# Kernel optimization log

Measured on AMD Instinct MI355X. Metric: run time of the kernel, lower is better.

The kernel has to match this reference:

```python
import jax, jax.numpy as jnp
import numpy as np

N, E, FT_IN, HID, FT_OUT, H = 32768, 524288, 256, 256, 512, 4
C = HID // H  # per-head dim = 64


def gatv2_conv(x, edge_index, w_l, b_l, w_r, b_r, att, bias):
    """PyG GATv2Conv (eval mode, add_self_loops=True, concat=True)."""
    n = x.shape[0]
    loop = jnp.arange(n)
    src = jnp.concatenate([edge_index[0], loop])  # j (source / neighbor)
    dst = jnp.concatenate([edge_index[1], loop])  # i (target)
    x_l = (x @ w_l + b_l).reshape(n, H, C)
    x_r = (x @ w_r + b_r).reshape(n, H, C)
    e = jax.nn.leaky_relu(x_l[src] + x_r[dst], 0.2)        # [E+N, H, C]
    logits = jnp.einsum('ehc,hc->eh', e, att)              # [E+N, H]
    m = jax.ops.segment_max(logits, dst, num_segments=n)
    m = jnp.where(jnp.isfinite(m), m, 0.0)
    p = jnp.exp(logits - m[dst])
    s = jax.ops.segment_sum(p, dst, num_segments=n)
    alpha = p / (s[dst] + 1e-16)                           # scatter-softmax over in-edges
    out = jax.ops.segment_sum(alpha[:, :, None] * x_l[src], dst, num_segments=n)
    return out.reshape(n, H * C) + bias


def gelu(x):
    return jax.nn.gelu(x, approximate=False)  # torch nn.GELU default (erf)


def setup_inputs() -> dict:
    key = jax.random.key(0)
    ks = jax.random.split(key, 24)
    sc = lambda fan_in: 1.0 / np.sqrt(fan_in)
    d = {
        'x': jax.random.normal(ks[0], (N, FT_IN), jnp.float32),
        'edge_index': jax.random.randint(ks[1], (2, E), 0, N, dtype=jnp.int32),
        'batch': jnp.repeat(jnp.arange(64, dtype=jnp.int32), N // 64),
        'batch_size': 64,
        # conv1 params
        'w1_l': jax.random.normal(ks[2], (FT_IN, HID), jnp.float32) * sc(FT_IN),
        'b1_l': jnp.zeros((HID,), jnp.float32),
        'w1_r': jax.random.normal(ks[3], (FT_IN, HID), jnp.float32) * sc(FT_IN),
        'b1_r': jnp.zeros((HID,), jnp.float32),
        'att1': jax.random.normal(ks[4], (H, C), jnp.float32) * sc(C),
        'bias1': jnp.zeros((HID,), jnp.float32),
        # conv2 params
        'w2_l': jax.random.normal(ks[5], (HID, HID), jnp.float32) * sc(HID),
        'b2_l': jnp.zeros((HID,), jnp.float32),
        'w2_r': jax.random.normal(ks[6], (HID, HID), jnp.float32) * sc(HID),
        'b2_r': jnp.zeros((HID,), jnp.float32),
        'att2': jax.random.normal(ks[7], (H, C), jnp.float32) * sc(C),
        'bias2': jnp.zeros((HID,), jnp.float32),
        # MLP head
        'lin1_w': jax.random.normal(ks[8], (HID, 4 * HID), jnp.float32) * sc(HID),
        'lin1_b': jnp.zeros((4 * HID,), jnp.float32),
        'lin2_w': jax.random.normal(ks[9], (4 * HID, HID), jnp.float32) * sc(4 * HID),
        'lin2_b': jnp.zeros((HID,), jnp.float32),
        'fin_w': jax.random.normal(ks[10], (HID, FT_OUT), jnp.float32) * sc(HID),
        'fin_b': jnp.zeros((FT_OUT,), jnp.float32),
    }
    return d


def reference(x, edge_index, batch, batch_size,
              w1_l, b1_l, w1_r, b1_r, att1, bias1,
              w2_l, b2_l, w2_r, b2_r, att2, bias2,
              lin1_w, lin1_b, lin2_w, lin2_b, fin_w, fin_b):
    h = gatv2_conv(x, edge_index, w1_l, b1_l, w1_r, b1_r, att1, bias1)
    h = gelu(h)
    h = gatv2_conv(h, edge_index, w2_l, b2_l, w2_r, b2_r, att2, bias2)
    # global mean pool per graph
    n_graphs = batch_size
    sums = jax.ops.segment_sum(h, batch, num_segments=n_graphs)
    cnts = jax.ops.segment_sum(jnp.ones((h.shape[0],), h.dtype), batch, num_segments=n_graphs)
    graph_mean = sums / jnp.maximum(cnts, 1.0)[:, None]
    # take node 0 of each graph (dropouts are identity in eval)
    z = h.reshape(batch_size, -1, HID)[:, 0, :]
    z = gelu(z @ lin1_w + lin1_b) @ lin2_w + lin2_b
    z = z @ fin_w + fin_b
    return z, graph_mean
```

## Files before the change

kernel.cpp:

```cpp
#include <hip/hip_runtime.h>
#include <hip/hip_bf16.h>
#include <stdint.h>

typedef __attribute__((ext_vector_type(8))) short short8;
typedef __attribute__((ext_vector_type(4))) float floatx4;
typedef __attribute__((ext_vector_type(2))) float floatx2;
typedef __attribute__((ext_vector_type(2))) int intx2;
typedef __hip_bfloat16 bf16;

__device__ __forceinline__ float b2f(bf16 v) { return __bfloat162float(v); }
__device__ __forceinline__ bf16 f2b(float v) { return __float2bfloat16(v); }
__device__ __forceinline__ float gelu_f(float v) {
    return 0.5f * v * (1.0f + erff(v * 0.70710678118654752f));
}
__device__ __forceinline__ floatx2 cvt2(unsigned v) {
    floatx2 r;
    r.x = __uint_as_float(v << 16);
    r.y = __uint_as_float(v & 0xffff0000u);
    return r;
}
template <int CTRL>
__device__ __forceinline__ float dpp_add(float v) {
    int x = __builtin_amdgcn_update_dpp(0, __float_as_int(v), CTRL, 0xf, 0xf, true);
    return v + __int_as_float(x);
}
__device__ __forceinline__ float sum_halves(float v) {
#if __has_builtin(__builtin_amdgcn_permlane32_swap)
    intx2 r = __builtin_amdgcn_permlane32_swap(__float_as_int(v), __float_as_int(v),
                                               false, false);
    return __int_as_float(r.x) + __int_as_float(r.y);
#else
    return v + __shfl_xor(v, 32, 64);
#endif
}

#define GLD_LDS16(gptr, lptr) \
  __builtin_amdgcn_global_load_lds((const __attribute__((address_space(1))) void*)(gptr), \
                                   (__attribute__((address_space(3))) void*)(lptr), 16, 0, 0)


__global__ void k_tr_scatter(const int* __restrict__ dst, const int* __restrict__ src,
                             int* __restrict__ cnt, int* __restrict__ col, int E,
                             const float* __restrict__ Wl1, const float* __restrict__ Wr1,
                             const float* __restrict__ Wl2, const float* __restrict__ Wr2,
                             bf16* __restrict__ Wt,
                             const float* __restrict__ x, bf16* __restrict__ xb) {
    int bx = blockIdx.x;
    if (bx < 512) {
        int g = bx * 256 + threadIdx.x;
        if (g * 4 < E) {
            int4 d = ((const int4*)dst)[g];
            int4 s = ((const int4*)src)[g];
            int rk;
            rk = atomicAdd(&cnt[d.x], 1); if (rk < 64) col[(d.x << 6) + rk] = s.x;
            rk = atomicAdd(&cnt[d.y], 1); if (rk < 64) col[(d.y << 6) + rk] = s.y;
            rk = atomicAdd(&cnt[d.z], 1); if (rk < 64) col[(d.z << 6) + rk] = s.z;
            rk = atomicAdd(&cnt[d.w], 1); if (rk < 64) col[(d.w << 6) + rk] = s.w;
        }
    } else if (bx < 1536) {
        int b = bx - 512;
        int r = b & 255, half = (b >> 8) & 1, layer = b >> 9;
        int c = threadIdx.x;
        const float* W = layer ? (half ? Wr2 : Wl2) : (half ? Wr1 : Wl1);
        Wt[(size_t)(layer * 512 + half * 256 + c) * 256 + r] = f2b(W[r * 256 + c]);
    } else {
        int b = bx - 1536;
        size_t base = ((size_t)b * 256 + threadIdx.x) * 32;
        const float4* xin = (const float4*)(x + base);
        #pragma unroll
        for (int q = 0; q < 4; q++) {
            float4 a = xin[2 * q];
            float4 c = xin[2 * q + 1];
            bf16 t[8] = {f2b(a.x), f2b(a.y), f2b(a.z), f2b(a.w),
                         f2b(c.x), f2b(c.y), f2b(c.z), f2b(c.w)};
            *(short8*)(xb + base + q * 8) = *(const short8*)t;
        }
    }
}

__global__ __launch_bounds__(256) void k_gemm(const bf16* __restrict__ A,
                                              const bf16* __restrict__ Bt,
                                              const float* __restrict__ biasL,
                                              const float* __restrict__ biasR,
                                              bf16* __restrict__ C, int K) {
    __shared__ bf16 smem[16384];
    bf16* As = smem;
    bf16* Bs = smem + 8192;
    const int n0 = blockIdx.x * 128;
    const int m0 = blockIdx.y * 128;
    const int tid  = threadIdx.x;
    const int wave = tid >> 6;
    const int lane = tid & 63;
    const int quad = lane >> 4;
    const int l16  = lane & 15;
    const int wm = (wave & 1) * 64;
    const int wn = (wave >> 1) * 64;
    const int scole = ((lane & 7) ^ (lane >> 3)) * 8;
    const int srow  = lane >> 3;

    floatx4 acc[4][4] = {};

    for (int k0 = 0; k0 < K; k0 += 64) {
        #pragma unroll
        for (int i = 0; i < 4; i++) {
            int chunk = i * 4 + wave;
            int row = chunk * 8 + srow;
            GLD_LDS16(A + (size_t)(m0 + row) * K + k0 + scole,
                      (char*)As + chunk * 1024 + lane * 16);
            GLD_LDS16(Bt + (size_t)(n0 + row) * K + k0 + scole,
                      (char*)Bs + chunk * 1024 + lane * 16);
        }
        __syncthreads();
        #pragma unroll
        for (int ks = 0; ks < 2; ks++) {
            short8 af[4], bfr[4];
            int pk = ((ks * 4 + quad) ^ (l16 & 7)) * 8;
            #pragma unroll
            for (int i = 0; i < 4; i++) {
                af[i]  = *(const short8*)&As[(wm + i * 16 + l16) * 64 + pk];
                bfr[i] = *(const short8*)&Bs[(wn + i * 16 + l16) * 64 + pk];
            }
            #pragma unroll
            for (int i = 0; i < 4; i++)
                #pragma unroll
                for (int j = 0; j < 4; j++)
                    acc[i][j] = __builtin_amdgcn_mfma_f32_16x16x32_bf16(af[i], bfr[j], acc[i][j], 0, 0, 0);
        }
        __syncthreads();
    }

    float bvj[4];
    #pragma unroll
    for (int j = 0; j < 4; j++) {
        int gcol = n0 + wn + j * 16 + l16;
        bvj[j] = (gcol < 256) ? biasL[gcol] : biasR[gcol - 256];
    }
    #pragma unroll
    for (int h = 0; h < 2; h++) {
        if ((wave & 1) == h) {
            #pragma unroll
            for (int j = 0; j < 4; j++) {
                int lcol = wn + j * 16 + l16;
                #pragma unroll
                for (int i = 0; i < 4; i++)
                    #pragma unroll
                    for (int r = 0; r < 4; r++)
                        smem[(i * 16 + quad * 4 + r) * 136 + lcol] = f2b(acc[i][j][r] + bvj[j]);
            }
        }
        __syncthreads();
        {
            int rl = tid >> 4;
            int cs = (tid & 15) * 8;
            #pragma unroll
            for (int p = 0; p < 4; p++) {
                int row = p * 16 + rl;
                short8 v = *(const short8*)&smem[row * 136 + cs];
                *(short8*)(C + (size_t)(m0 + h * 64 + row) * 512 + n0 + cs) = v;
            }
        }
        if (h == 0) __syncthreads();
    }
}

__global__ __launch_bounds__(128) void k_agg(const bf16* __restrict__ xlr,
                                             const float* __restrict__ att,
                                             const int* __restrict__ cnt,
                                             const int* __restrict__ col,
                                             const float* __restrict__ bias,
                                             bf16* __restrict__ out, int do_gelu) {
    int wave = threadIdx.x >> 6, lane = threadIdx.x & 63;
    int i = blockIdx.x * 2 + wave;
    int hl = lane & 31;
    int half = lane >> 5;
    unsigned f = (hl >> 3) * 64 + (hl & 7) * 8;

    const float LOG2E = 1.4426950408889634f;
    const floatx2 c02 = {0.2f, 0.2f};
    floatx2 attv[4], xrv[4];
    {
        floatx4 a0 = *(const floatx4*)(att + f);
        floatx4 a1 = *(const floatx4*)(att + f + 4);
        attv[0] = (floatx2){LOG2E * a0[0], LOG2E * a0[1]};
        attv[1] = (floatx2){LOG2E * a0[2], LOG2E * a0[3]};
        attv[2] = (floatx2){LOG2E * a1[0], LOG2E * a1[1]};
        attv[3] = (floatx2){LOG2E * a1[2], LOG2E * a1[3]};
        unsigned raw[4];
        *(uint4*)raw = *(const uint4*)(xlr + ((unsigned)i * 512u + 256u + f));
        #pragma unroll
        for (int k = 0; k < 4; k++) xrv[k] = cvt2(raw[k]);
    }

    int deg = cnt[i];
    deg = deg > 64 ? 64 : deg;
    int e0 = i << 6;
    int total = 1 + deg;

    int src_c = i;
    if (half == 1 && total > 1) src_c = col[e0];
    unsigned g_cur[4];
    *(uint4*)g_cur = *(const uint4*)(xlr + ((unsigned)src_c * 512u + f));
    int t1 = 2 + half;
    int src_n = (t1 < total) ? col[e0 + t1 - 1] : i;

    float s = 0.f;
    floatx2 acc2[4] = {};

    for (int base = 0; base < total; base += 2) {
        unsigned g_nxt[4];
        *(uint4*)g_nxt = *(const uint4*)(xlr + ((unsigned)src_n * 512u + f));
        int t2 = base + 4 + half;
        int src_n2 = (t2 < total) ? col[e0 + t2 - 1] : i;
        bool valid = (base + half) < total;
        floatx2 xv[4], l2 = {0.f, 0.f};
        #pragma unroll
        for (int k = 0; k < 4; k++) {
            xv[k] = cvt2(g_cur[k]);
            floatx2 u = xv[k] + xrv[k];
            floatx2 lr = __builtin_elementwise_max(u, u * c02);
            l2 += lr * attv[k];
        }
        float l = l2.x + l2.y;
        l = dpp_add<0xB1>(l);
        l = dpp_add<0x4E>(l);
        l = dpp_add<0x141>(l);
        float p;
        asm("v_exp_f32 %0, %1" : "=v"(p) : "v"(l));
        p = valid ? p : 0.f;
        s += p;
        floatx2 p2 = {p, p};
        #pragma unroll
        for (int k = 0; k < 4; k++) acc2[k] += p2 * xv[k];
        #pragma unroll
        for (int k = 0; k < 4; k++) g_cur[k] = g_nxt[k];
        src_n = src_n2;
    }

    s = sum_halves(s);
    #pragma unroll
    for (int k = 0; k < 4; k++) {
        acc2[k].x = sum_halves(acc2[k].x);
        acc2[k].y = sum_halves(acc2[k].y);
    }

    if (half == 0) {
        float inv = 1.0f / (s + 1e-16f);
        bf16 ov[8];
        #pragma unroll
        for (int k = 0; k < 4; k++) {
            float v0 = acc2[k].x * inv + bias[f + 2 * k];
            float v1 = acc2[k].y * inv + bias[f + 2 * k + 1];
            if (do_gelu) { v0 = gelu_f(v0); v1 = gelu_f(v1); }
            ov[2 * k]     = f2b(v0);
            ov[2 * k + 1] = f2b(v1);
        }
        *(short8*)(out + ((unsigned)i * 256u + f)) = *(const short8*)ov;
    }
}

__device__ __forceinline__ void head_body(const bf16* __restrict__ inB,
                                          const float* __restrict__ inF,
                                          const float* __restrict__ W,
                                          const float* __restrict__ bias,
                                          float* __restrict__ out,
                                          int K, int N, long long row_stride, int act,
                                          int g, int chunk, float* zin, float* red) {
    int t = threadIdx.x;
    int nc = t & 63;
    int kq = t >> 6;
    int n = chunk * 64 + nc;
    for (int k = t; k < K; k += 256)
        zin[k] = inB ? b2f(inB[(size_t)g * row_stride + k])
                     : inF[(size_t)g * row_stride + k];
    __syncthreads();
    const int klen = K >> 2;
    const int kb = kq * klen;
    float acc = 0.f;
    #pragma unroll 8
    for (int k = 0; k < klen; k++)
        acc = fmaf(zin[kb + k], W[(size_t)(kb + k) * N + n], acc);
    red[t] = acc;
    __syncthreads();
    if (kq == 0) {
        float v = red[nc] + red[nc + 64] + red[nc + 128] + red[nc + 192] + bias[n];
        if (act) v = gelu_f(v);
        out[(size_t)g * N + n] = v;
    }
}

__global__ __launch_bounds__(256) void k_pe1(const bf16* __restrict__ hb,
                                             float* __restrict__ part,
                                             const float* __restrict__ lin1w,
                                             const float* __restrict__ lin1b,
                                             float* __restrict__ t1, int PG) {
    __shared__ float zin[256];
    __shared__ float red[256];
    int bx = blockIdx.x;
    if (bx < 512) {
        int g = bx >> 3, p = bx & 7, c = threadIdx.x;
        int rows_per = PG / 8;
        const bf16* base = hb + ((size_t)g * PG + (size_t)p * rows_per) * 256;
        float acc = 0.f;
        for (int r = 0; r < rows_per; r++) acc += b2f(base[(size_t)r * 256 + c]);
        part[((size_t)g * 8 + p) * 256 + c] = acc;
    } else {
        int b = bx - 512;
        head_body(hb, nullptr, lin1w, lin1b, t1, 256, 1024,
                  (long long)PG * 256, 1, b >> 4, b & 15, zin, red);
    }
}

__global__ __launch_bounds__(256) void k_pe2(const float* __restrict__ part,
                                             float* __restrict__ outPool, int PG,
                                             const float* __restrict__ t1,
                                             const float* __restrict__ lin2w,
                                             const float* __restrict__ lin2b,
                                             float* __restrict__ t2) {
    __shared__ float zin[1024];
    __shared__ float red[256];
    int bx = blockIdx.x;
    if (bx < 64) {
        int g = bx, c = threadIdx.x;
        float acc = 0.f;
        for (int p = 0; p < 8; p++) acc += part[((size_t)g * 8 + p) * 256 + c];
        outPool[g * 256 + c] = acc / (float)PG;
    } else {
        int b = bx - 64;
        head_body(nullptr, t1, lin2w, lin2b, t2, 1024, 256,
                  1024, 0, b >> 2, b & 3, zin, red);
    }
}

__global__ __launch_bounds__(256) void k_fin(const float* __restrict__ t2,
                                             const float* __restrict__ finw,
                                             const float* __restrict__ finb,
                                             float* __restrict__ out) {
    __shared__ float zin[256];
    __shared__ float red[256];
    head_body(nullptr, t2, finw, finb, out, 256, 512,
              256, 0, blockIdx.x, blockIdx.y, zin, red);
}

extern "C" void kernel_launch(void* const* d_in, const int* in_sizes, int n_in,
                              void* d_out, int out_size, void* d_ws, size_t ws_size,
                              hipStream_t stream) {
    const float* x     = (const float*)d_in[0];
    const int*   ei    = (const int*)d_in[1];
    const float* w1_l  = (const float*)d_in[4];
    const float* b1_l  = (const float*)d_in[5];
    const float* w1_r  = (const float*)d_in[6];
    const float* b1_r  = (const float*)d_in[7];
    const float* att1  = (const float*)d_in[8];
    const float* bias1 = (const float*)d_in[9];
    const float* w2_l  = (const float*)d_in[10];
    const float* b2_l  = (const float*)d_in[11];
    const float* w2_r  = (const float*)d_in[12];
    const float* b2_r  = (const float*)d_in[13];
    const float* att2  = (const float*)d_in[14];
    const float* bias2 = (const float*)d_in[15];
    const float* lin1w = (const float*)d_in[16];
    const float* lin1b = (const float*)d_in[17];
    const float* lin2w = (const float*)d_in[18];
    const float* lin2b = (const float*)d_in[19];
    const float* finw  = (const float*)d_in[20];
    const float* finb  = (const float*)d_in[21];

    const int N  = in_sizes[0] / 256;
    const int E  = in_sizes[1] / 2;
    const int NG = 64;
    const int PG = N / NG;

    char* ws = (char*)d_ws;
    size_t off = 0;
    bf16* xlr = (bf16*)(ws + off); off += (size_t)N * 512 * 2;
    bf16* hb  = (bf16*)(ws + off); off += (size_t)N * 256 * 2;
    bf16* wt  = (bf16*)(ws + off); off += 2 * 512 * 256 * 2;
    int* cnt  = (int*)(ws + off); off += (size_t)N * 4;
    int* col  = (int*)(ws + off); off += (size_t)N * 64 * 4;
    float* pws = (float*)(ws + off); off += (size_t)NG * 8 * 256 * 4;
    float* t1  = (float*)(ws + off); off += (size_t)NG * 1024 * 4;
    float* t2  = (float*)(ws + off); off += (size_t)NG * 256 * 4;

    bf16* xb = hb;

    const int* srcv = ei;
    const int* dstv = ei + E;

    hipMemsetAsync(cnt, 0, (size_t)N * 4, stream);
    k_tr_scatter<<<512 + 1024 + 1024, 256, 0, stream>>>(dstv, srcv, cnt, col, E,
                                                        w1_l, w1_r, w2_l, w2_r, wt,
                                                        x, xb);

    dim3 gg(4, N / 128);
    k_gemm<<<gg, 256, 0, stream>>>(xb, wt, b1_l, b1_r, xlr, 256);
    k_agg<<<N / 2, 128, 0, stream>>>(xlr, att1, cnt, col, bias1, hb, 1);

    k_gemm<<<gg, 256, 0, stream>>>(hb, wt + 512 * 256, b2_l, b2_r, xlr, 256);
    k_agg<<<N / 2, 128, 0, stream>>>(xlr, att2, cnt, col, bias2, hb, 0);

    float* outp = (float*)d_out;
    k_pe1<<<512 + 1024, 256, 0, stream>>>(hb, pws, lin1w, lin1b, t1, PG);
    k_pe2<<<64 + 256, 256, 0, stream>>>(pws, outp + 64 * 512, PG, t1, lin2w, lin2b, t2);
    dim3 gf(NG, 512 / 64);
    k_fin<<<gf, 256, 0, stream>>>(t2, finw, finb, outp);
}
```

Measured before the change: 324.7 us.

## Overlap CSR edge scatter with first GEMM and fold memset into prep kernel

Moves the atomic edge-scatter that builds the per-destination neighbor lists out of the prep kernel and into the first-layer GEMM launch, interleaving one scatter block with every two GEMM blocks. The atomic-bound scatter then overlaps with the compute-bound GEMM instead of running serially. The memset of the count array is also replaced by extra blocks in the prep kernel, removing one launch. Scatter blocks now reserve the GEMM's shared memory, which may lower occupancy for those blocks.

```diff
diff --git a/kernel.cpp b/kernel.cpp
--- a/kernel.cpp
+++ b/kernel.cpp
@@ -39,32 +39,19 @@
                                    (__attribute__((address_space(3))) void*)(lptr), 16, 0, 0)
 
 
-__global__ void k_tr_scatter(const int* __restrict__ dst, const int* __restrict__ src,
-                             int* __restrict__ cnt, int* __restrict__ col, int E,
-                             const float* __restrict__ Wl1, const float* __restrict__ Wr1,
-                             const float* __restrict__ Wl2, const float* __restrict__ Wr2,
-                             bf16* __restrict__ Wt,
-                             const float* __restrict__ x, bf16* __restrict__ xb) {
+__global__ void k_tr(const float* __restrict__ Wl1, const float* __restrict__ Wr1,
+                     const float* __restrict__ Wl2, const float* __restrict__ Wr2,
+                     bf16* __restrict__ Wt,
+                     const float* __restrict__ x, bf16* __restrict__ xb,
+                     int* __restrict__ cnt) {
     int bx = blockIdx.x;
-    if (bx < 512) {
-        int g = bx * 256 + threadIdx.x;
-        if (g * 4 < E) {
-            int4 d = ((const int4*)dst)[g];
-            int4 s = ((const int4*)src)[g];
-            int rk;
-            rk = atomicAdd(&cnt[d.x], 1); if (rk < 64) col[(d.x << 6) + rk] = s.x;
-            rk = atomicAdd(&cnt[d.y], 1); if (rk < 64) col[(d.y << 6) + rk] = s.y;
-            rk = atomicAdd(&cnt[d.z], 1); if (rk < 64) col[(d.z << 6) + rk] = s.z;
-            rk = atomicAdd(&cnt[d.w], 1); if (rk < 64) col[(d.w << 6) + rk] = s.w;
-        }
-    } else if (bx < 1536) {
-        int b = bx - 512;
-        int r = b & 255, half = (b >> 8) & 1, layer = b >> 9;
+    if (bx < 1024) {
+        int r = bx & 255, half = (bx >> 8) & 1, layer = bx >> 9;
         int c = threadIdx.x;
         const float* W = layer ? (half ? Wr2 : Wl2) : (half ? Wr1 : Wl1);
         Wt[(size_t)(layer * 512 + half * 256 + c) * 256 + r] = f2b(W[r * 256 + c]);
-    } else {
-        int b = bx - 1536;
+    } else if (bx < 2048) {
+        int b = bx - 1024;
         size_t base = ((size_t)b * 256 + threadIdx.x) * 32;
         const float4* xin = (const float4*)(x + base);
         #pragma unroll
@@ -75,19 +62,20 @@
                          f2b(c.x), f2b(c.y), f2b(c.z), f2b(c.w)};
             *(short8*)(xb + base + q * 8) = *(const short8*)t;
         }
-    }
-}
-
-__global__ __launch_bounds__(256) void k_gemm(const bf16* __restrict__ A,
-                                              const bf16* __restrict__ Bt,
-                                              const float* __restrict__ biasL,
-                                              const float* __restrict__ biasR,
-                                              bf16* __restrict__ C, int K) {
-    __shared__ bf16 smem[16384];
+    } else {
+        cnt[(bx - 2048) * 256 + threadIdx.x] = 0;
+    }
+}
+
+__device__ __forceinline__ void gemm_body(const bf16* __restrict__ A,
+                                          const bf16* __restrict__ Bt,
+                                          const float* __restrict__ biasL,
+                                          const float* __restrict__ biasR,
+                                          bf16* __restrict__ C,
+                                          int K, int m0, int n0,
+                                          bf16* __restrict__ smem) {
     bf16* As = smem;
     bf16* Bs = smem + 8192;
-    const int n0 = blockIdx.x * 128;
-    const int m0 = blockIdx.y * 128;
     const int tid  = threadIdx.x;
     const int wave = tid >> 6;
     const int lane = tid & 63;
@@ -161,6 +149,46 @@
         }
         if (h == 0) __syncthreads();
     }
+}
+
+__global__ __launch_bounds__(256) void k_scatter_gemm(const int* __restrict__ src,
+                                                      const int* __restrict__ dst,
+                                                      int* __restrict__ cnt,
+                                                      int* __restrict__ col, int E,
+                                                      const bf16* __restrict__ A,
+                                                      const bf16* __restrict__ Bt,
+                                                      const float* __restrict__ biasL,
+                                                      const float* __restrict__ biasR,
+                                                      bf16* __restrict__ C, int K) {
+    __shared__ bf16 smem[16384];
+    int bx = blockIdx.x;
+    int rem = bx % 3;
+    if (rem == 2) {
+        int g = (bx / 3) * 256 + threadIdx.x;
+        if (g * 4 < E) {
+            int4 d = ((const int4*)dst)[g];
+            int4 s = ((const int4*)src)[g];
+            int rk;
+            rk = atomicAdd(&cnt[d.x], 1); if (rk < 64) col[(d.x << 6) + rk] = s.x;
+            rk = atomicAdd(&cnt[d.y], 1); if (rk < 64) col[(d.y << 6) + rk] = s.y;
+            rk = atomicAdd(&cnt[d.z], 1); if (rk < 64) col[(d.z << 6) + rk] = s.z;
+            rk = atomicAdd(&cnt[d.w], 1); if (rk < 64) col[(d.w << 6) + rk] = s.w;
+        }
+    } else {
+        int gid = (bx / 3) * 2 + rem;
+        int n0 = (gid & 3) * 128;
+        int m0 = (gid >> 2) * 128;
+        gemm_body(A, Bt, biasL, biasR, C, K, m0, n0, smem);
+    }
+}
+
+__global__ __launch_bounds__(256) void k_gemm2(const bf16* __restrict__ A,
+                                               const bf16* __restrict__ Bt,
+                                               const float* __restrict__ biasL,
+                                               const float* __restrict__ biasR,
+                                               bf16* __restrict__ C, int K) {
+    __shared__ bf16 smem[16384];
+    gemm_body(A, Bt, biasL, biasR, C, K, blockIdx.y * 128, blockIdx.x * 128, smem);
 }
 
 __global__ __launch_bounds__(128) void k_agg(const bf16* __restrict__ xlr,
@@ -386,16 +414,14 @@
     const int* srcv = ei;
     const int* dstv = ei + E;
 
-    hipMemsetAsync(cnt, 0, (size_t)N * 4, stream);
-    k_tr_scatter<<<512 + 1024 + 1024, 256, 0, stream>>>(dstv, srcv, cnt, col, E,
-                                                        w1_l, w1_r, w2_l, w2_r, wt,
-                                                        x, xb);
+    k_tr<<<1024 + 1024 + 128, 256, 0, stream>>>(w1_l, w1_r, w2_l, w2_r, wt, x, xb, cnt);
+
+    k_scatter_gemm<<<512 + 1024, 256, 0, stream>>>(srcv, dstv, cnt, col, E,
+                                                   xb, wt, b1_l, b1_r, xlr, 256);
+    k_agg<<<N / 2, 128, 0, stream>>>(xlr, att1, cnt, col, bias1, hb, 1);
 
     dim3 gg(4, N / 128);
-    k_gemm<<<gg, 256, 0, stream>>>(xb, wt, b1_l, b1_r, xlr, 256);
-    k_agg<<<N / 2, 128, 0, stream>>>(xlr, att1, cnt, col, bias1, hb, 1);
-
-    k_gemm<<<gg, 256, 0, stream>>>(hb, wt + 512 * 256, b2_l, b2_r, xlr, 256);
+    k_gemm2<<<gg, 256, 0, stream>>>(hb, wt + 512 * 256, b2_l, b2_r, xlr, 256);
     k_agg<<<N / 2, 128, 0, stream>>>(xlr, att2, cnt, col, bias2, hb, 0);
 
     float* outp = (float*)d_out;
```

After: 298.4 us. 8.1% less time.
